# Performance work log

Hardware: AMD Instinct MI355X
Metric: run time of the kernel (lower is better)

The kernel has to match this reference:

```python
import jax, jax.numpy as jnp
import numpy as np
import math

B, T, D = 2, 2048, 1024
H = 16
HD = D // H
DFF = 4096
EPS = 1e-5


def setup_inputs() -> dict:
    key = jax.random.key(0)
    ks = jax.random.split(key, 11)
    s = 0.02
    return {
        "x": jax.random.normal(ks[0], (B, T, D), dtype=jnp.float32),
        "scale1": jnp.ones((D,), jnp.float32),
        "scale2": jnp.ones((D,), jnp.float32),
        "Wqkv": jax.random.normal(ks[1], (D, 3 * D), jnp.float32) * s,
        "bqkv": jnp.zeros((3 * D,), jnp.float32),
        "Wo": jax.random.normal(ks[2], (D, D), jnp.float32) * s,
        "bo": jnp.zeros((D,), jnp.float32),
        "W1": jax.random.normal(ks[3], (D, DFF), jnp.float32) * s,
        "b1": jnp.zeros((DFF,), jnp.float32),
        "W2": jax.random.normal(ks[4], (DFF, D), jnp.float32) * s,
        "b2": jnp.zeros((D,), jnp.float32),
    }


def rmsnorm(x, scale):
    # Faithful to source: norm = ||x||/sqrt(d); out = scale * x / (norm + eps)
    d = x.shape[-1]
    norm = jnp.linalg.norm(x, axis=-1, keepdims=True) * (1.0 / math.sqrt(d))
    return scale * x / (norm + EPS)


def attention(x, Wqkv, bqkv, Wo, bo):
    b, t, c = x.shape
    qkv = x @ Wqkv + bqkv                       # [B,T,3D]
    qkv = qkv.reshape(b, t, 3, H, HD)
    q, k, v = qkv[:, :, 0], qkv[:, :, 1], qkv[:, :, 2]   # [B,T,H,HD]
    scores = jnp.einsum("bqhd,bkhd->bhqk", q, k) / math.sqrt(HD)
    w = jax.nn.softmax(scores, axis=-1)
    out = jnp.einsum("bhqk,bkhd->bqhd", w, v).reshape(b, t, c)
    return out @ Wo + bo


def reference(x, scale1, scale2, Wqkv, bqkv, Wo, bo, W1, b1, W2, b2):
    x = x + attention(rmsnorm(x, scale1), Wqkv, bqkv, Wo, bo)
    h = rmsnorm(x, scale2)
    ff = (jax.nn.gelu(h @ W1 + b1, approximate=False)) @ W2 + b2
    return x + ff
```

## Files before the change

### kernel.cpp

```cpp
#include <hip/hip_runtime.h>
#include <hip/hip_bf16.h>
#include <math.h>

typedef unsigned short u16;
typedef __bf16 bf16x8 __attribute__((ext_vector_type(8)));
typedef float f32x4 __attribute__((ext_vector_type(4)));
typedef unsigned int u32x2 __attribute__((ext_vector_type(2)));

#define B_   2
#define T_   2048
#define D_   1024
#define H_   16
#define HD_  64
#define DFF_ 4096
#define M_TOK (B_*T_)

__device__ __forceinline__ u16 f2bf(float f){
  unsigned u = __float_as_uint(f);
  u += 0x7fff + ((u>>16)&1);
  return (u16)(u>>16);
}

__device__ __forceinline__ void gl2lds16(const void* g, void* l){
  __builtin_amdgcn_global_load_lds((const __attribute__((address_space(1))) void*)g,
                                   (__attribute__((address_space(3))) void*)l, 16, 0, 0);
}

__device__ __forceinline__ unsigned lds_u32(const void* p){
  return (unsigned)(uintptr_t)(const __attribute__((address_space(3))) void*)p;
}

__device__ __forceinline__ u32x2 tr_read(unsigned addr){
  u32x2 d;
  asm volatile("ds_read_b64_tr_b16 %0, %1" : "=v"(d) : "v"(addr));
  return d;
}
__device__ __forceinline__ u32x2 tr_read512(unsigned addr){
  u32x2 d;
  asm volatile("ds_read_b64_tr_b16 %0, %1 offset:512" : "=v"(d) : "v"(addr));
  return d;
}
__device__ __forceinline__ bf16x8 pack8(u32x2 a, u32x2 b){
  union { u32x2 u[2]; bf16x8 v; } x; x.u[0]=a; x.u[1]=b; return x.v;
}

__global__ __launch_bounds__(256) void k_transpose_bf16(const float* __restrict__ in,
                                                        u16* __restrict__ out, int K, int N){
  __shared__ float t[32][33];
  int bx = blockIdx.x*32, by = blockIdx.y*32;
  int tx = threadIdx.x, ty = threadIdx.y;
  #pragma unroll
  for(int i=ty;i<32;i+=8) t[i][tx] = in[(size_t)(by+i)*N + bx + tx];
  __syncthreads();
  #pragma unroll
  for(int i=ty;i<32;i+=8) out[(size_t)(bx+i)*K + by + tx] = f2bf(t[tx][i]);
}

__global__ __launch_bounds__(256) void k_rmsnorm_bf16(const float* __restrict__ x,
                                                      const float* __restrict__ scale,
                                                      u16* __restrict__ out){
  int row = blockIdx.x;
  int tid = threadIdx.x;
  int lane = tid&63, wave = tid>>6;
  const float4* xr = (const float4*)(x + (size_t)row*D_);
  float4 v = xr[tid];
  float ss = v.x*v.x + v.y*v.y + v.z*v.z + v.w*v.w;
  #pragma unroll
  for(int o=1;o<64;o<<=1) ss += __shfl_xor(ss, o);
  __shared__ float red[4];
  if(lane==0) red[wave]=ss;
  __syncthreads();
  float tot = red[0]+red[1]+red[2]+red[3];
  float inv = 1.0f/(sqrtf(tot*(1.0f/D_)) + 1e-5f);
  const float4* sr = (const float4*)scale;
  float4 s4 = sr[tid];
  u16* o4 = out + (size_t)row*D_ + tid*4;
  o4[0]=f2bf(v.x*s4.x*inv); o4[1]=f2bf(v.y*s4.y*inv);
  o4[2]=f2bf(v.z*s4.z*inv); o4[3]=f2bf(v.w*s4.w*inv);
}

template<int EPI>
__global__ __launch_bounds__(256) void k_gemm(const u16* __restrict__ A, const u16* __restrict__ Bt,
                                              const float* __restrict__ bias, const float* __restrict__ res,
                                              void* __restrict__ Cout, int M, int N, int K){
  __shared__ u16 As[128*32];
  __shared__ u16 Bs[128*32];
  int tid = threadIdx.x;
  int lane = tid&63, wave = tid>>6;
  int wr = wave>>1, wc = wave&1;
  int row0 = blockIdx.x*128, col0 = blockIdx.y*128;
  f32x4 acc[4][4];
  #pragma unroll
  for(int m=0;m<4;m++)
    #pragma unroll
    for(int n=0;n<4;n++) acc[m][n] = (f32x4){0.f,0.f,0.f,0.f};
  const u16* Ag = A + (size_t)row0*K;
  const u16* Bg = Bt + (size_t)col0*K;
  for(int k0=0;k0<K;k0+=32){
    __syncthreads();
    #pragma unroll
    for(int c=tid;c<512;c+=256){
      gl2lds16(Ag + (size_t)(c>>2)*K + k0 + (c&3)*8, (char*)As + c*16);
      gl2lds16(Bg + (size_t)(c>>2)*K + k0 + (c&3)*8, (char*)Bs + c*16);
    }
    __syncthreads();
    const u16* ab = As + (wr*64 + (lane&15))*32 + (lane>>4)*8;
    const u16* bb = Bs + (wc*64 + (lane&15))*32 + (lane>>4)*8;
    bf16x8 a[4], b[4];
    #pragma unroll
    for(int m=0;m<4;m++) a[m] = *(const bf16x8*)(ab + m*16*32);
    #pragma unroll
    for(int n=0;n<4;n++) b[n] = *(const bf16x8*)(bb + n*16*32);
    #pragma unroll
    for(int m=0;m<4;m++)
      #pragma unroll
      for(int n=0;n<4;n++)
        acc[m][n] = __builtin_amdgcn_mfma_f32_16x16x32_bf16(a[m], b[n], acc[m][n], 0,0,0);
  }
  #pragma unroll
  for(int m=0;m<4;m++){
    #pragma unroll
    for(int n=0;n<4;n++){
      #pragma unroll
      for(int r=0;r<4;r++){
        int row = row0 + wr*64 + m*16 + (lane>>4)*4 + r;
        int col = col0 + wc*64 + n*16 + (lane&15);
        float v = acc[m][n][r] + bias[col];
        if constexpr(EPI==1){
          ((float*)Cout)[(size_t)row*N + col] = v + res[(size_t)row*N + col];
        } else if constexpr(EPI==2){
          v = 0.5f*v*(1.0f + erff(v*0.70710678118f));
          ((u16*)Cout)[(size_t)row*N + col] = f2bf(v);
        } else {
          ((u16*)Cout)[(size_t)row*N + col] = f2bf(v);
        }
      }
    }
  }
}

__global__ __launch_bounds__(256,4) void k_attn(const u16* __restrict__ qkv, u16* __restrict__ O){
  __shared__ alignas(16) u16 Ks[2][4096];
  __shared__ alignas(16) u16 Vs[2][4096];
  __shared__ alignas(16) u16 Ps[4][1024];
  const int qt = blockIdx.x, h = blockIdx.y, b = blockIdx.z;
  const int tid = threadIdx.x, lane = tid&63, wave = tid>>6;
  const int lo = lane&15, hi = lane>>4, l7 = lane&7;
  const u16* qkvB = qkv + (size_t)b*T_*3072;
  const int hoff = h*64;

  const int q0 = qt*64 + wave*16;
  const u16* qp = qkvB + (size_t)(q0+lo)*3072 + hoff + hi*8;
  bf16x8 aq0 = *(const bf16x8*)qp;
  bf16x8 aq1 = *(const bf16x8*)(qp+32);

  size_t sK[2], sV[2];
  {
    int cc[2] = {tid, tid+256};
    #pragma unroll
    for(int i=0;i<2;i++){
      int c = cc[i];
      sK[i] = (size_t)(c>>3)*3072 + 1024 + hoff + (((c&7)^((c>>3)&7))<<3);
      int kv = ((c>>5)<<2) + ((c>>1)&3);
      int d0 = (((c&31)>>3)<<4) | ((c&1)<<3);
      sV[i] = (size_t)kv*3072 + 2048 + hoff + d0;
    }
  }
  const unsigned kb0 = (unsigned)lo*128 + (unsigned)((hi^l7))*16;
  const unsigned kb1 = (unsigned)lo*128 + (unsigned)(((hi|4)^l7))*16;
  const unsigned vtr = (unsigned)hi*1024 + (unsigned)lo*2;

  f32x4 oac[4];
  #pragma unroll
  for(int n=0;n<4;n++) oac[n] = (f32x4){0.f,0.f,0.f,0.f};
  float mrow[4] = {-1e30f,-1e30f,-1e30f,-1e30f};
  float lrow[4] = {0.f,0.f,0.f,0.f};

  {
    char* kd = (char*)Ks[0]; char* vd = (char*)Vs[0];
    gl2lds16(qkvB + sK[0], kd + tid*16);
    gl2lds16(qkvB + sK[1], kd + tid*16 + 4096);
    gl2lds16(qkvB + sV[0], vd + tid*16);
    gl2lds16(qkvB + sV[1], vd + tid*16 + 4096);
  }
  int buf = 0;
  for(int t=0;t<T_/64;t++){
    __syncthreads();
    if(t < T_/64-1){
      size_t koff = (size_t)(t+1)*64*3072;
      char* kd = (char*)Ks[buf^1]; char* vd = (char*)Vs[buf^1];
      gl2lds16(qkvB + koff + sK[0], kd + tid*16);
      gl2lds16(qkvB + koff + sK[1], kd + tid*16 + 4096);
      gl2lds16(qkvB + koff + sV[0], vd + tid*16);
      gl2lds16(qkvB + koff + sV[1], vd + tid*16 + 4096);
    }
    const char* K_ = (const char*)Ks[buf];
    u16* P_ = Ps[wave];

    f32x4 s[4];
    #pragma unroll
    for(int n=0;n<4;n++){
      bf16x8 b0 = *(const bf16x8*)(K_ + n*2048 + kb0);
      bf16x8 b1 = *(const bf16x8*)(K_ + n*2048 + kb1);
      f32x4 z = (f32x4){0.f,0.f,0.f,0.f};
      z = __builtin_amdgcn_mfma_f32_16x16x32_bf16(aq0, b0, z, 0,0,0);
      z = __builtin_amdgcn_mfma_f32_16x16x32_bf16(aq1, b1, z, 0,0,0);
      s[n] = z;
    }

    float mx[4]; int ok = 1;
    #pragma unroll
    for(int r=0;r<4;r++){
      mx[r] = fmaxf(fmaxf(s[0][r],s[1][r]),fmaxf(s[2][r],s[3][r]));
      ok &= (mx[r] <= mrow[r] + 64.0f) ? 1 : 0;
    }
    if(!__all(ok)){
      #pragma unroll
      for(int r=0;r<4;r++){
        float mm = mx[r];
        mm = fmaxf(mm, __shfl_xor(mm,1));
        mm = fmaxf(mm, __shfl_xor(mm,2));
        mm = fmaxf(mm, __shfl_xor(mm,4));
        mm = fmaxf(mm, __shfl_xor(mm,8));
        float nm = fmaxf(mrow[r], mm);
        float alpha = __expf((mrow[r]-nm)*0.125f);
        mrow[r] = nm;
        lrow[r] *= alpha;
        #pragma unroll
        for(int n=0;n<4;n++) oac[n][r] *= alpha;
      }
    }
    #pragma unroll
    for(int r=0;r<4;r++){
      float p[4];
      #pragma unroll
      for(int n=0;n<4;n++) p[n] = __expf((s[n][r]-mrow[r])*0.125f);
      lrow[r] += (p[0]+p[1])+(p[2]+p[3]);
      const int q = hi*4 + r;
      const unsigned X = (unsigned)(q&7)<<4;
      char* pb = (char*)P_ + q*128;
      #pragma unroll
      for(int n=0;n<4;n++)
        *(u16*)(pb + (((unsigned)(lo*2 + n*32))^X)) = f2bf(p[n]);
    }

    const unsigned vsb = lds_u32(Vs[buf]);
    #pragma unroll
    for(int kk=0;kk<2;kk++){
      bf16x8 ap = *(const bf16x8*)((const char*)P_ + (kk==0 ? kb0 : kb1));
      u32x2 t0[4], t1[4];
      #pragma unroll
      for(int n=0;n<4;n++){
        unsigned a = vsb + vtr + (unsigned)kk*4096 + (unsigned)n*128;
        t0[n] = tr_read(a);
        t1[n] = tr_read512(a);
      }
      asm volatile("s_waitcnt lgkmcnt(0)" ::: "memory");
      __builtin_amdgcn_sched_barrier(0);
      #pragma unroll
      for(int n=0;n<4;n++){
        bf16x8 bv = pack8(t0[n], t1[n]);
        oac[n] = __builtin_amdgcn_mfma_f32_16x16x32_bf16(ap, bv, oac[n], 0,0,0);
      }
    }
    buf ^= 1;
  }

  #pragma unroll
  for(int r=0;r<4;r++){
    float lr = lrow[r];
    lr += __shfl_xor(lr,1);
    lr += __shfl_xor(lr,2);
    lr += __shfl_xor(lr,4);
    lr += __shfl_xor(lr,8);
    lrow[r] = 1.0f/lr;
  }
  size_t obase = ((size_t)b*T_ + q0)*D_ + hoff;
  #pragma unroll
  for(int n=0;n<4;n++)
    #pragma unroll
    for(int r=0;r<4;r++)
      O[obase + (size_t)(hi*4+r)*D_ + n*16 + lo] = f2bf(oac[n][r]*lrow[r]);
}

extern "C" void kernel_launch(void* const* d_in, const int* in_sizes, int n_in,
                              void* d_out, int out_size, void* d_ws, size_t ws_size,
                              hipStream_t stream){
  (void)in_sizes; (void)n_in; (void)out_size; (void)ws_size;
  const float* x      = (const float*)d_in[0];
  const float* scale1 = (const float*)d_in[1];
  const float* scale2 = (const float*)d_in[2];
  const float* Wqkv   = (const float*)d_in[3];
  const float* bqkv   = (const float*)d_in[4];
  const float* Wo     = (const float*)d_in[5];
  const float* bo     = (const float*)d_in[6];
  const float* W1     = (const float*)d_in[7];
  const float* b1     = (const float*)d_in[8];
  const float* W2     = (const float*)d_in[9];
  const float* b2     = (const float*)d_in[10];
  float* out = (float*)d_out;

  char* w = (char*)d_ws;
  u16* xn1   = (u16*)w;  w += (size_t)M_TOK*D_*2;
  u16* qkvb  = (u16*)w;  w += (size_t)M_TOK*3*D_*2;
  u16* Obuf  = (u16*)w;  w += (size_t)M_TOK*D_*2;
  float* x2  = (float*)w; w += (size_t)M_TOK*D_*4;
  u16* xn2   = (u16*)w;  w += (size_t)M_TOK*D_*2;
  u16* h1    = (u16*)w;  w += (size_t)M_TOK*DFF_*2;
  u16* Wqkvt = (u16*)w;  w += (size_t)3*D_*D_*2;
  u16* Wot   = (u16*)w;  w += (size_t)D_*D_*2;
  u16* W1t   = (u16*)w;  w += (size_t)D_*DFF_*2;
  u16* W2t   = (u16*)w;  w += (size_t)DFF_*D_*2;

  dim3 tb(32,8);
  k_transpose_bf16<<<dim3(3*D_/32, D_/32), tb, 0, stream>>>(Wqkv, Wqkvt, D_, 3*D_);
  k_transpose_bf16<<<dim3(D_/32,   D_/32), tb, 0, stream>>>(Wo,   Wot,   D_, D_);
  k_transpose_bf16<<<dim3(DFF_/32, D_/32), tb, 0, stream>>>(W1,   W1t,   D_, DFF_);
  k_transpose_bf16<<<dim3(D_/32, DFF_/32), tb, 0, stream>>>(W2,   W2t,   DFF_, D_);

  k_rmsnorm_bf16<<<M_TOK, 256, 0, stream>>>(x, scale1, xn1);
  k_gemm<0><<<dim3(M_TOK/128, 3*D_/128), 256, 0, stream>>>(xn1, Wqkvt, bqkv, nullptr, qkvb, M_TOK, 3*D_, D_);
  k_attn<<<dim3(T_/64, H_, B_), 256, 0, stream>>>(qkvb, Obuf);
  k_gemm<1><<<dim3(M_TOK/128, D_/128), 256, 0, stream>>>(Obuf, Wot, bo, x, x2, M_TOK, D_, D_);
  k_rmsnorm_bf16<<<M_TOK, 256, 0, stream>>>(x2, scale2, xn2);
  k_gemm<2><<<dim3(M_TOK/128, DFF_/128), 256, 0, stream>>>(xn2, W1t, b1, nullptr, h1, M_TOK, DFF_, D_);
  k_gemm<1><<<dim3(M_TOK/128, D_/128), 256, 0, stream>>>(h1, W2t, b2, x2, out, M_TOK, D_, DFF_);
}
```

Measured before the change: 301.2 us.

## Pipeline GEMM k-loop with 4-stage LDS ring buffer and XOR swizzle

Replaces the GEMM's single-buffered load-then-compute loop with a 4-deep LDS ring. Async global-to-LDS loads run three tiles ahead, gated by explicit vmcnt waits and one barrier per k-step. It also XOR-swizzles the 16-byte chunks within each row to cut LDS bank conflicts on the fragment reads. The aim is to hide global memory latency behind MFMA work, at the cost of four times the LDS per block, which may reduce occupancy.

```diff
diff --git a/kernel.cpp b/kernel.cpp
--- a/kernel.cpp
+++ b/kernel.cpp
@@ -42,6 +42,13 @@
 }
 __device__ __forceinline__ bf16x8 pack8(u32x2 a, u32x2 b){
   union { u32x2 u[2]; bf16x8 v; } x; x.u[0]=a; x.u[1]=b; return x.v;
+}
+
+__device__ __forceinline__ void block_barrier(){
+  asm volatile("" ::: "memory");
+  __builtin_amdgcn_s_barrier();
+  __builtin_amdgcn_sched_barrier(0);
+  asm volatile("" ::: "memory");
 }
 
 __global__ __launch_bounds__(256) void k_transpose_bf16(const float* __restrict__ in,
@@ -83,10 +90,11 @@
 __global__ __launch_bounds__(256) void k_gemm(const u16* __restrict__ A, const u16* __restrict__ Bt,
                                               const float* __restrict__ bias, const float* __restrict__ res,
                                               void* __restrict__ Cout, int M, int N, int K){
-  __shared__ u16 As[128*32];
-  __shared__ u16 Bs[128*32];
+  __shared__ u16 As[4][4096];
+  __shared__ u16 Bs[4][4096];
   int tid = threadIdx.x;
   int lane = tid&63, wave = tid>>6;
+  int lo = lane&15, hi = lane>>4;
   int wr = wave>>1, wc = wave&1;
   int row0 = blockIdx.x*128, col0 = blockIdx.y*128;
   f32x4 acc[4][4];
@@ -96,35 +104,66 @@
     for(int n=0;n<4;n++) acc[m][n] = (f32x4){0.f,0.f,0.f,0.f};
   const u16* Ag = A + (size_t)row0*K;
   const u16* Bg = Bt + (size_t)col0*K;
-  for(int k0=0;k0<K;k0+=32){
-    __syncthreads();
-    #pragma unroll
-    for(int c=tid;c<512;c+=256){
-      gl2lds16(Ag + (size_t)(c>>2)*K + k0 + (c&3)*8, (char*)As + c*16);
-      gl2lds16(Bg + (size_t)(c>>2)*K + k0 + (c&3)*8, (char*)Bs + c*16);
-    }
-    __syncthreads();
-    const u16* ab = As + (wr*64 + (lane&15))*32 + (lane>>4)*8;
-    const u16* bb = Bs + (wc*64 + (lane&15))*32 + (lane>>4)*8;
+
+  size_t soff[2];
+  {
+    int cc[2] = {tid, tid+256};
+    #pragma unroll
+    for(int i=0;i<2;i++){
+      int c = cc[i];
+      soff[i] = (size_t)(c>>2)*K + (size_t)((((c&3) ^ ((c>>2)&3)))<<3);
+    }
+  }
+  const int NT = K>>5;
+
+  #define STAGE_G(t) { \
+    const u16* Ab = Ag + (size_t)(t)*32; const u16* Bb = Bg + (size_t)(t)*32; \
+    char* ad = (char*)As[(t)&3]; char* bd = (char*)Bs[(t)&3]; \
+    gl2lds16(Ab + soff[0], ad + tid*16); \
+    gl2lds16(Ab + soff[1], ad + tid*16 + 4096); \
+    gl2lds16(Bb + soff[0], bd + tid*16); \
+    gl2lds16(Bb + soff[1], bd + tid*16 + 4096); \
+  }
+
+  auto compute = [&](int t){
+    const char* ab = (const char*)As[t&3] + (wr*64+lo)*64;
+    const char* bb = (const char*)Bs[t&3] + (wc*64+lo)*64;
+    const unsigned sw = (unsigned)((hi^(lo&3))*16);
     bf16x8 a[4], b[4];
     #pragma unroll
-    for(int m=0;m<4;m++) a[m] = *(const bf16x8*)(ab + m*16*32);
-    #pragma unroll
-    for(int n=0;n<4;n++) b[n] = *(const bf16x8*)(bb + n*16*32);
+    for(int m=0;m<4;m++) a[m] = *(const bf16x8*)(ab + m*1024 + sw);
+    #pragma unroll
+    for(int n=0;n<4;n++) b[n] = *(const bf16x8*)(bb + n*1024 + sw);
     #pragma unroll
     for(int m=0;m<4;m++)
       #pragma unroll
       for(int n=0;n<4;n++)
         acc[m][n] = __builtin_amdgcn_mfma_f32_16x16x32_bf16(a[m], b[n], acc[m][n], 0,0,0);
-  }
+  };
+
+  STAGE_G(0); STAGE_G(1); STAGE_G(2);
+  for(int t=0;t<NT-2;t++){
+    asm volatile("s_waitcnt vmcnt(8)" ::: "memory");
+    block_barrier();
+    if(t+3 < NT) STAGE_G(t+3);
+    compute(t);
+  }
+  asm volatile("s_waitcnt vmcnt(4)" ::: "memory");
+  block_barrier();
+  compute(NT-2);
+  asm volatile("s_waitcnt vmcnt(0)" ::: "memory");
+  block_barrier();
+  compute(NT-1);
+  #undef STAGE_G
+
   #pragma unroll
   for(int m=0;m<4;m++){
     #pragma unroll
     for(int n=0;n<4;n++){
       #pragma unroll
       for(int r=0;r<4;r++){
-        int row = row0 + wr*64 + m*16 + (lane>>4)*4 + r;
-        int col = col0 + wc*64 + n*16 + (lane&15);
+        int row = row0 + wr*64 + m*16 + hi*4 + r;
+        int col = col0 + wc*64 + n*16 + lo;
         float v = acc[m][n][r] + bias[col];
         if constexpr(EPI==1){
           ((float*)Cout)[(size_t)row*N + col] = v + res[(size_t)row*N + col];
```

Result: slower. 311.8 us (+3.5%).

## Split-K the FF2 GEMM with a reduce epilogue and raise attention MFMA priority

Applied to the files above, without the earlier changes.

The final FF2 GEMM (K=4096) is split into two K halves across a third grid dimension. Each half writes fp32 partials into a workspace region that aliases buffers already dead by that point (xn1 and qkv). A separate elementwise kernel then sums the two partials and adds bias and residual. This doubles the block count so the 256-block grid is not one thin wave, but it adds roughly 32MB of partial writes plus a reduce pass, and it uses a simpler single-buffered GEMM loop. Separately, the attention kernel raises wave priority around its MFMA bursts with s_setprio to favour matrix issue over other waves.

```diff
diff --git a/kernel.cpp b/kernel.cpp
--- a/kernel.cpp
+++ b/kernel.cpp
@@ -139,6 +139,78 @@
   }
 }
 
+__global__ __launch_bounds__(256) void k_gemm_pk(const u16* __restrict__ A, const u16* __restrict__ Bt,
+                                                 float* __restrict__ P, int M, int N, int K){
+  __shared__ u16 As[128*32];
+  __shared__ u16 Bs[128*32];
+  int tid = threadIdx.x;
+  int lane = tid&63, wave = tid>>6;
+  int wr = wave>>1, wc = wave&1;
+  int row0 = blockIdx.x*128, col0 = blockIdx.y*128;
+  int kc = blockIdx.z;
+  int klen = K/2, kbeg = kc*klen;
+  f32x4 acc[4][4];
+  #pragma unroll
+  for(int m=0;m<4;m++)
+    #pragma unroll
+    for(int n=0;n<4;n++) acc[m][n] = (f32x4){0.f,0.f,0.f,0.f};
+  const u16* Ag = A + (size_t)row0*K + kbeg;
+  const u16* Bg = Bt + (size_t)col0*K + kbeg;
+  for(int k0=0;k0<klen;k0+=32){
+    __syncthreads();
+    #pragma unroll
+    for(int c=tid;c<512;c+=256){
+      gl2lds16(Ag + (size_t)(c>>2)*K + k0 + (c&3)*8, (char*)As + c*16);
+      gl2lds16(Bg + (size_t)(c>>2)*K + k0 + (c&3)*8, (char*)Bs + c*16);
+    }
+    __syncthreads();
+    const u16* ab = As + (wr*64 + (lane&15))*32 + (lane>>4)*8;
+    const u16* bb = Bs + (wc*64 + (lane&15))*32 + (lane>>4)*8;
+    bf16x8 a[4], b[4];
+    #pragma unroll
+    for(int m=0;m<4;m++) a[m] = *(const bf16x8*)(ab + m*16*32);
+    #pragma unroll
+    for(int n=0;n<4;n++) b[n] = *(const bf16x8*)(bb + n*16*32);
+    #pragma unroll
+    for(int m=0;m<4;m++)
+      #pragma unroll
+      for(int n=0;n<4;n++)
+        acc[m][n] = __builtin_amdgcn_mfma_f32_16x16x32_bf16(a[m], b[n], acc[m][n], 0,0,0);
+  }
+  float* Pk = P + (size_t)kc*M*N;
+  #pragma unroll
+  for(int m=0;m<4;m++)
+    #pragma unroll
+    for(int n=0;n<4;n++)
+      #pragma unroll
+      for(int r=0;r<4;r++){
+        int row = row0 + wr*64 + m*16 + (lane>>4)*4 + r;
+        int col = col0 + wc*64 + n*16 + (lane&15);
+        Pk[(size_t)row*N + col] = acc[m][n][r];
+      }
+}
+
+__global__ __launch_bounds__(256) void k_ff2_reduce(const float* __restrict__ P,
+                                                    const float* __restrict__ bias,
+                                                    const float* __restrict__ res,
+                                                    float* __restrict__ out){
+  const size_t total4 = (size_t)M_TOK*D_/4;
+  const float4* p0 = (const float4*)P;
+  const float4* p1 = (const float4*)(P + (size_t)M_TOK*D_);
+  const float4* rr = (const float4*)res;
+  const float4* bb = (const float4*)bias;
+  float4* oo = (float4*)out;
+  for(size_t i = (size_t)blockIdx.x*256 + threadIdx.x; i < total4; i += (size_t)gridDim.x*256){
+    float4 a = p0[i], b = p1[i], r = rr[i], c = bb[i & (D_/4 - 1)];
+    float4 o;
+    o.x = (a.x+b.x)+(c.x+r.x);
+    o.y = (a.y+b.y)+(c.y+r.y);
+    o.z = (a.z+b.z)+(c.z+r.z);
+    o.w = (a.w+b.w)+(c.w+r.w);
+    oo[i] = o;
+  }
+}
+
 __global__ __launch_bounds__(256,4) void k_attn(const u16* __restrict__ qkv, u16* __restrict__ O){
   __shared__ alignas(16) u16 Ks[2][4096];
   __shared__ alignas(16) u16 Vs[2][4096];
@@ -198,6 +270,7 @@
     u16* P_ = Ps[wave];
 
     f32x4 s[4];
+    __builtin_amdgcn_s_setprio(1);
     #pragma unroll
     for(int n=0;n<4;n++){
       bf16x8 b0 = *(const bf16x8*)(K_ + n*2048 + kb0);
@@ -207,6 +280,7 @@
       z = __builtin_amdgcn_mfma_f32_16x16x32_bf16(aq1, b1, z, 0,0,0);
       s[n] = z;
     }
+    __builtin_amdgcn_s_setprio(0);
 
     float mx[4]; int ok = 1;
     #pragma unroll
@@ -257,11 +331,13 @@
       }
       asm volatile("s_waitcnt lgkmcnt(0)" ::: "memory");
       __builtin_amdgcn_sched_barrier(0);
+      __builtin_amdgcn_s_setprio(1);
       #pragma unroll
       for(int n=0;n<4;n++){
         bf16x8 bv = pack8(t0[n], t1[n]);
         oac[n] = __builtin_amdgcn_mfma_f32_16x16x32_bf16(ap, bv, oac[n], 0,0,0);
       }
+      __builtin_amdgcn_s_setprio(0);
     }
     buf ^= 1;
   }
@@ -311,6 +387,7 @@
   u16* Wot   = (u16*)w;  w += (size_t)D_*D_*2;
   u16* W1t   = (u16*)w;  w += (size_t)D_*DFF_*2;
   u16* W2t   = (u16*)w;  w += (size_t)DFF_*D_*2;
+  float* pk  = (float*)d_ws;
 
   dim3 tb(32,8);
   k_transpose_bf16<<<dim3(3*D_/32, D_/32), tb, 0, stream>>>(Wqkv, Wqkvt, D_, 3*D_);
@@ -324,5 +401,6 @@
   k_gemm<1><<<dim3(M_TOK/128, D_/128), 256, 0, stream>>>(Obuf, Wot, bo, x, x2, M_TOK, D_, D_);
   k_rmsnorm_bf16<<<M_TOK, 256, 0, stream>>>(x2, scale2, xn2);
   k_gemm<2><<<dim3(M_TOK/128, DFF_/128), 256, 0, stream>>>(xn2, W1t, b1, nullptr, h1, M_TOK, DFF_, D_);
-  k_gemm<1><<<dim3(M_TOK/128, D_/128), 256, 0, stream>>>(h1, W2t, b2, x2, out, M_TOK, D_, DFF_);
-}
+  k_gemm_pk<<<dim3(M_TOK/128, D_/128, 2), 256, 0, stream>>>(h1, W2t, pk, M_TOK, D_, DFF_);
+  k_ff2_reduce<<<2048, 256, 0, stream>>>(pk, b2, x2, out);
+}
```

Measured after the change: 285.4 us. 5.2% less time.
